# Performance work log

Hardware: AMD Instinct MI355X
Metric: run time of the kernel (lower is better)

## Reference

```python
import jax, jax.numpy as jnp
import numpy as np

N_NODES = 100000
N_EDGES = 3200000
F_IN = 128
HID = 32
N_CLASSES = 40
NEG_SLOPE = 0.2


def _add_self_loops(edge_index, n):
    loops = jnp.arange(n, dtype=edge_index.dtype)
    src = jnp.concatenate([edge_index[0], loops])
    dst = jnp.concatenate([edge_index[1], loops])
    return src, dst


def _gat_layer(x, src, dst, W, a_src, a_dst, b, n):
    # h: [N, C]
    h = x @ W
    hs = h[src]                      # [E, C] gathered source features
    alpha_s = hs @ a_src             # [E]
    alpha_d = (h @ a_dst)[dst]       # [E]
    e = jax.nn.leaky_relu(alpha_s + alpha_d, NEG_SLOPE)
    # segment softmax over incoming edges per destination node
    m = jax.ops.segment_max(e, dst, num_segments=n)
    ex = jnp.exp(e - m[dst])
    denom = jax.ops.segment_sum(ex, dst, num_segments=n)
    alpha = ex / denom[dst]
    out = jax.ops.segment_sum(alpha[:, None] * hs, dst, num_segments=n)
    return out + b


def setup_inputs() -> dict:
    key = jax.random.key(0)
    ks = jax.random.split(key, 8)
    x = jax.random.normal(ks[0], (N_NODES, F_IN), dtype=jnp.float32)
    edge_index = jax.random.randint(ks[1], (2, N_EDGES), 0, N_NODES, dtype=jnp.int32)
    W1 = jax.random.normal(ks[2], (F_IN, HID), dtype=jnp.float32) * (1.0 / np.sqrt(F_IN))
    att_src1 = jax.random.normal(ks[3], (HID,), dtype=jnp.float32) * 0.1
    att_dst1 = jax.random.normal(ks[4], (HID,), dtype=jnp.float32) * 0.1
    b1 = jnp.zeros((HID,), dtype=jnp.float32)
    W2 = jax.random.normal(ks[5], (HID, N_CLASSES), dtype=jnp.float32) * (1.0 / np.sqrt(HID))
    att_src2 = jax.random.normal(ks[6], (N_CLASSES,), dtype=jnp.float32) * 0.1
    att_dst2 = jax.random.normal(ks[7], (N_CLASSES,), dtype=jnp.float32) * 0.1
    b2 = jnp.zeros((N_CLASSES,), dtype=jnp.float32)
    return {"x": x, "edge_index": edge_index, "W1": W1, "att_src1": att_src1,
            "att_dst1": att_dst1, "b1": b1, "W2": W2, "att_src2": att_src2,
            "att_dst2": att_dst2, "b2": b2}


def reference(x, edge_index, W1, att_src1, att_dst1, b1, W2, att_src2, att_dst2, b2):
    n = x.shape[0]
    src, dst = _add_self_loops(edge_index, n)  # PyG GATConv default add_self_loops=True
    h = _gat_layer(x, src, dst, W1, att_src1, att_dst1, b1, n)
    h = jax.nn.relu(h)  # dropout is identity in eval mode
    h = _gat_layer(h, src, dst, W2, att_src2, att_dst2, b2, n)
    h = jax.nn.relu(h)
    return jax.nn.log_softmax(h, axis=1)
```

## Files before the change

kernel.cpp:

```cpp
#include <hip/hip_runtime.h>
#include <hip/hip_bf16.h>
#include <hip/hip_fp16.h>
#include <math.h>

#define N_NODES 100000
#define N_EDGES 3200000
#define ET (N_EDGES + N_NODES)
#define F_IN 128
#define HID 32
#define NCLS 40
#define NEG 0.2f

#define NB 782
#define CHUNK 4096
#define NBLK 782
#define BCAP 5120
#define NB1 299
#define GROWS 64
#define GEMM_BLKS ((N_NODES + GROWS - 1) / GROWS)

#define BSUM_SCAN(bscan, bsums)                                                   \
    if (t < 64) {                                                                 \
        int base5 = t * 5;                                                        \
        int bv0 = (base5     < NB1) ? bsums[base5]     : 0;                       \
        int bv1 = (base5 + 1 < NB1) ? bsums[base5 + 1] : 0;                       \
        int bv2 = (base5 + 2 < NB1) ? bsums[base5 + 2] : 0;                       \
        int bv3 = (base5 + 3 < NB1) ? bsums[base5 + 3] : 0;                       \
        int bv4 = (base5 + 4 < NB1) ? bsums[base5 + 4] : 0;                       \
        int bs = bv0 + bv1 + bv2 + bv3 + bv4;                                     \
        int brun = bs;                                                            \
        for (int boff = 1; boff < 64; boff <<= 1) {                               \
            int bx = __shfl_up(brun, boff);                                       \
            if (t >= boff) brun += bx;                                            \
        }                                                                         \
        brun -= bs;                                                               \
        if (base5     < NB1) { bscan[base5]     = brun; brun += bv0; }            \
        if (base5 + 1 < NB1) { bscan[base5 + 1] = brun; brun += bv1; }            \
        if (base5 + 2 < NB1) { bscan[base5 + 2] = brun; brun += bv2; }            \
        if (base5 + 3 < NB1) { bscan[base5 + 3] = brun; brun += bv3; }            \
        if (base5 + 4 < NB1) { bscan[base5 + 4] = brun; }                         \
    }

__global__ __launch_bounds__(256) void k_hist_gemm(
    const int* __restrict__ dst, int* __restrict__ Hm,
    const float* __restrict__ x, const float* __restrict__ W1,
    const float* __restrict__ a_s, const float* __restrict__ a_d,
    __half* __restrict__ h1h, float* __restrict__ s1, float* __restrict__ d1,
    const float* __restrict__ W2, const float* __restrict__ as2,
    const float* __restrict__ ad2, float* __restrict__ va_s, float* __restrict__ va_d) {
    __shared__ __align__(16) float Ws[F_IN * HID];
    int t = threadIdx.x;
    if (blockIdx.x < NBLK) {
        int* hist = (int*)Ws;
        int k = blockIdx.x;
        for (int i = t; i < NB; i += 256) hist[i] = 0;
        __syncthreads();
        int b4 = k * (CHUNK / 4);
#pragma unroll
        for (int j = 0; j < CHUNK / 4 / 256; j++) {
            int i4 = b4 + j * 256 + t;
            if (i4 < N_EDGES / 4) {
                int4 d = ((const int4*)dst)[i4];
                atomicAdd(&hist[d.x >> 7], 1);
                atomicAdd(&hist[d.y >> 7], 1);
                atomicAdd(&hist[d.z >> 7], 1);
                atomicAdd(&hist[d.w >> 7], 1);
            }
        }
        __syncthreads();
        for (int i = t; i < NB; i += 256) Hm[i * NBLK + k] = hist[i];
    } else if (blockIdx.x < NBLK + GEMM_BLKS) {
        int bb = blockIdx.x - NBLK;
        const float4* W4 = (const float4*)W1;
        float4* Ws4 = (float4*)Ws;
#pragma unroll
        for (int i = 0; i < F_IN * HID / 4 / 256; i++)
            Ws4[t + i * 256] = W4[t + i * 256];
        __syncthreads();
        int rp = t >> 3;
        int cq = t & 7;
        size_t v0 = (size_t)bb * GROWS + rp * 2;
        size_t v1 = v0 + 1;
        size_t r0c = (v0 < N_NODES) ? v0 : (size_t)(N_NODES - 1);
        size_t r1c = (v1 < N_NODES) ? v1 : (size_t)(N_NODES - 1);
        const float4* xa4 = (const float4*)(x + r0c * F_IN);
        const float4* xb4 = (const float4*)(x + r1c * F_IN);
        const float4* Wc4 = (const float4*)Ws;
        float a00 = 0.f, a01 = 0.f, a02 = 0.f, a03 = 0.f;
        float a10 = 0.f, a11 = 0.f, a12 = 0.f, a13 = 0.f;
#pragma unroll
        for (int k4 = 0; k4 < F_IN / 4; k4++) {
            float4 xa = xa4[k4];
            float4 xb = xb4[k4];
            int kb = k4 * 4;
            float4 w0 = Wc4[(kb + 0) * 8 + cq];
            float4 w1 = Wc4[(kb + 1) * 8 + cq];
            float4 w2 = Wc4[(kb + 2) * 8 + cq];
            float4 w3 = Wc4[(kb + 3) * 8 + cq];
            a00 = fmaf(xa.x, w0.x, a00); a01 = fmaf(xa.x, w0.y, a01);
            a02 = fmaf(xa.x, w0.z, a02); a03 = fmaf(xa.x, w0.w, a03);
            a00 = fmaf(xa.y, w1.x, a00); a01 = fmaf(xa.y, w1.y, a01);
            a02 = fmaf(xa.y, w1.z, a02); a03 = fmaf(xa.y, w1.w, a03);
            a00 = fmaf(xa.z, w2.x, a00); a01 = fmaf(xa.z, w2.y, a01);
            a02 = fmaf(xa.z, w2.z, a02); a03 = fmaf(xa.z, w2.w, a03);
            a00 = fmaf(xa.w, w3.x, a00); a01 = fmaf(xa.w, w3.y, a01);
            a02 = fmaf(xa.w, w3.z, a02); a03 = fmaf(xa.w, w3.w, a03);
            a10 = fmaf(xb.x, w0.x, a10); a11 = fmaf(xb.x, w0.y, a11);
            a12 = fmaf(xb.x, w0.z, a12); a13 = fmaf(xb.x, w0.w, a13);
            a10 = fmaf(xb.y, w1.x, a10); a11 = fmaf(xb.y, w1.y, a11);
            a12 = fmaf(xb.y, w1.z, a12); a13 = fmaf(xb.y, w1.w, a13);
            a10 = fmaf(xb.z, w2.x, a10); a11 = fmaf(xb.z, w2.y, a11);
            a12 = fmaf(xb.z, w2.z, a12); a13 = fmaf(xb.z, w2.w, a13);
            a10 = fmaf(xb.w, w3.x, a10); a11 = fmaf(xb.w, w3.y, a11);
            a12 = fmaf(xb.w, w3.z, a12); a13 = fmaf(xb.w, w3.w, a13);
        }
        if (v0 < N_NODES) {
            __half2 p0 = __floats2half2_rn(a00, a01);
            __half2 p1 = __floats2half2_rn(a02, a03);
            uint2 u;
            u.x = *(const unsigned int*)&p0;
            u.y = *(const unsigned int*)&p1;
            *((uint2*)(h1h + v0 * HID + cq * 4)) = u;
        }
        if (v1 < N_NODES) {
            __half2 p0 = __floats2half2_rn(a10, a11);
            __half2 p1 = __floats2half2_rn(a12, a13);
            uint2 u;
            u.x = *(const unsigned int*)&p0;
            u.y = *(const unsigned int*)&p1;
            *((uint2*)(h1h + v1 * HID + cq * 4)) = u;
        }
        float4 asv = *(const float4*)(a_s + cq * 4);
        float4 adv = *(const float4*)(a_d + cq * 4);
        float p0s = a00 * asv.x + a01 * asv.y + a02 * asv.z + a03 * asv.w;
        float p0d = a00 * adv.x + a01 * adv.y + a02 * adv.z + a03 * adv.w;
        float p1s = a10 * asv.x + a11 * asv.y + a12 * asv.z + a13 * asv.w;
        float p1d = a10 * adv.x + a11 * adv.y + a12 * adv.z + a13 * adv.w;
#pragma unroll
        for (int off = 1; off <= 4; off <<= 1) {
            p0s += __shfl_xor(p0s, off); p0d += __shfl_xor(p0d, off);
            p1s += __shfl_xor(p1s, off); p1d += __shfl_xor(p1d, off);
        }
        if (cq == 0) {
            if (v0 < N_NODES) { s1[v0] = p0s; d1[v0] = p0d; }
            if (v1 < N_NODES) { s1[v1] = p1s; d1[v1] = p1d; }
        }
    } else {
        if (t < HID) {
            float ps = 0.f, pd = 0.f;
            for (int c = 0; c < NCLS; c++) {
                float w = W2[t * NCLS + c];
                ps = fmaf(w, as2[c], ps);
                pd = fmaf(w, ad2[c], pd);
            }
            va_s[t] = ps;
            va_d[t] = pd;
        }
    }
}

__global__ void k_scan_a(const int* __restrict__ in, int* __restrict__ out,
                         int* __restrict__ bsums, int L) {
    __shared__ int sd[256];
    int t = threadIdx.x, b = blockIdx.x;
    int base = b * 2048 + t * 8;
    int v[8];
    int ts = 0;
#pragma unroll
    for (int u = 0; u < 8; u++) {
        v[u] = (base + u < L) ? in[base + u] : 0;
        ts += v[u];
    }
    sd[t] = ts;
    __syncthreads();
    for (int off = 1; off < 256; off <<= 1) {
        int xx = (t >= off) ? sd[t - off] : 0;
        __syncthreads();
        sd[t] += xx;
        __syncthreads();
    }
    int run = sd[t] - ts;
    if (t == 255) bsums[b] = sd[255];
#pragma unroll
    for (int u = 0; u < 8; u++) {
        if (base + u < L) out[base + u] = run;
        run += v[u];
    }
}

__global__ __launch_bounds__(256) void kA_scatter(
    const int* __restrict__ src, const int* __restrict__ dst,
    const int* __restrict__ Sx, const int* __restrict__ bsums,
    unsigned int* __restrict__ tmp) {
    __shared__ int hist[NB];
    __shared__ int lofs[NB];
    __shared__ int tsum[256];
    __shared__ int bscan[NB1 + 1];
    __shared__ unsigned int stage[CHUNK];
    __shared__ unsigned short bkt16[CHUNK];
    int t = threadIdx.x, k = blockIdx.x;
    for (int i = t; i < NB; i += 256) hist[i] = 0;
    BSUM_SCAN(bscan, bsums)
    __syncthreads();
    int myd[16], mys[16];
    int b4 = k * (CHUNK / 4);
#pragma unroll
    for (int j = 0; j < CHUNK / 4 / 256; j++) {
        int i4 = b4 + j * 256 + t;
        if (i4 < N_EDGES / 4) {
            int4 d = ((const int4*)dst)[i4];
            int4 s = ((const int4*)src)[i4];
            myd[j * 4 + 0] = d.x; mys[j * 4 + 0] = s.x;
            myd[j * 4 + 1] = d.y; mys[j * 4 + 1] = s.y;
            myd[j * 4 + 2] = d.z; mys[j * 4 + 2] = s.z;
            myd[j * 4 + 3] = d.w; mys[j * 4 + 3] = s.w;
            atomicAdd(&hist[d.x >> 7], 1);
            atomicAdd(&hist[d.y >> 7], 1);
            atomicAdd(&hist[d.z >> 7], 1);
            atomicAdd(&hist[d.w >> 7], 1);
        } else {
#pragma unroll
            for (int u = 0; u < 4; u++) { myd[j * 4 + u] = -1; mys[j * 4 + u] = 0; }
        }
    }
    __syncthreads();
    int i0 = 4 * t;
    int h0 = (i0     < NB) ? hist[i0]     : 0;
    int h1 = (i0 + 1 < NB) ? hist[i0 + 1] : 0;
    int h2 = (i0 + 2 < NB) ? hist[i0 + 2] : 0;
    int h3 = (i0 + 3 < NB) ? hist[i0 + 3] : 0;
    int ts = h0 + h1 + h2 + h3;
    tsum[t] = ts;
    __syncthreads();
    for (int off = 1; off < 256; off <<= 1) {
        int xx = (t >= off) ? tsum[t - off] : 0;
        __syncthreads();
        tsum[t] += xx;
        __syncthreads();
    }
    int ex = tsum[t] - ts;
    if (i0     < NB) { lofs[i0]     = ex;                hist[i0]     = 0; }
    if (i0 + 1 < NB) { lofs[i0 + 1] = ex + h0;           hist[i0 + 1] = 0; }
    if (i0 + 2 < NB) { lofs[i0 + 2] = ex + h0 + h1;      hist[i0 + 2] = 0; }
    if (i0 + 3 < NB) { lofs[i0 + 3] = ex + h0 + h1 + h2; hist[i0 + 3] = 0; }
    __syncthreads();
#pragma unroll
    for (int j = 0; j < 16; j++) {
        if (myd[j] >= 0) {
            int bkt = myd[j] >> 7;
            int slot = lofs[bkt] + atomicAdd(&hist[bkt], 1);
            stage[slot] = ((unsigned int)(myd[j] & 127) << 17) | (unsigned int)mys[j];
            bkt16[slot] = (unsigned short)bkt;
        }
    }
    __syncthreads();
    for (int b = t; b < NB; b += 256) {
        int idx = b * NBLK + k;
        hist[b] = Sx[idx] + bscan[idx >> 11] - lofs[b];
    }
    __syncthreads();
    int nvalid = min(CHUNK, N_EDGES - k * CHUNK);
    for (int i = t; i < nvalid; i += 256)
        tmp[hist[bkt16[i]] + i] = stage[i];
}

__global__ __launch_bounds__(256) void kB_sort(
    const unsigned int* __restrict__ tmp, const int* __restrict__ Sx,
    const int* __restrict__ bsums,
    int* __restrict__ esrc, int* __restrict__ rs, int* __restrict__ deg) {
    __shared__ int ordered[BCAP + 128];
    __shared__ int cnt[128], lofs[128], cur[128], sc[128];
    __shared__ int bscan[NB1 + 1];
    int t = threadIdx.x, b = blockIdx.x;
    if (t < 128) { cnt[t] = 0; cur[t] = 0; }
    BSUM_SCAN(bscan, bsums)
    __syncthreads();
    int idx0 = b * NBLK;
    int myBase = Sx[idx0] + bscan[idx0 >> 11];
    int nextBase;
    if (b == NB - 1) nextBase = N_EDGES;
    else {
        int idx1 = (b + 1) * NBLK;
        nextBase = Sx[idx1] + bscan[idx1 >> 11];
    }
    int cntE = nextBase - myBase;
    int nNodes = min(128, N_NODES - b * 128);
    for (int i = t; i < cntE; i += 256) {
        unsigned int p = tmp[myBase + i];
        atomicAdd(&cnt[p >> 17], 1);
    }
    __syncthreads();
    int val = 0;
    if (t < 128) { val = (t < nNodes) ? cnt[t] + 1 : 0; sc[t] = val; }
    __syncthreads();
    for (int off = 1; off < 128; off <<= 1) {
        int xx = 0;
        if (t < 128 && t >= off) xx = sc[t - off];
        __syncthreads();
        if (t < 128) sc[t] += xx;
        __syncthreads();
    }
    if (t < 128) lofs[t] = sc[t] - val;
    __syncthreads();
    if (t < nNodes) ordered[lofs[t]] = b * 128 + t;
    for (int i = t; i < cntE; i += 256) {
        unsigned int p = tmp[myBase + i];
        int n = p >> 17;
        int slot = lofs[n] + 1 + atomicAdd(&cur[n], 1);
        ordered[slot] = (int)(p & 0x1FFFF);
    }
    __syncthreads();
    int gb = myBase + b * 128;
    int totOut = cntE + nNodes;
    for (int i = t; i < totOut; i += 256) esrc[gb + i] = ordered[i];
    if (t < nNodes) {
        rs[b * 128 + t] = gb + lofs[t];
        deg[b * 128 + t] = cnt[t] + 1;
    }
}

#define GATHER_BODY(SARR, TABLE)                                                  \
    float a0 = 0.f, a1 = 0.f, a2 = 0.f, a3 = 0.f,                                 \
          a4 = 0.f, a5 = 0.f, a6 = 0.f, a7 = 0.f;                                 \
    float den = 0.f;                                                              \
    int t = 0;                                                                    \
    for (; t + 16 <= cnt; t += 16) {                                              \
        int p0 = start + t + e;                                                   \
        int sa0 = esrc[p0];                                                       \
        int sa1 = esrc[p0 + 4];                                                   \
        int sa2 = esrc[p0 + 8];                                                   \
        int sa3 = esrc[p0 + 12];                                                  \
        float sv0 = SARR[sa0];                                                    \
        float sv1 = SARR[sa1];                                                    \
        float sv2 = SARR[sa2];                                                    \
        float sv3 = SARR[sa3];                                                    \
        uint4 hv0 = TABLE[(size_t)sa0 * 4 + q];                                   \
        uint4 hv1 = TABLE[(size_t)sa1 * 4 + q];                                   \
        uint4 hv2 = TABLE[(size_t)sa2 * 4 + q];                                   \
        uint4 hv3 = TABLE[(size_t)sa3 * 4 + q];                                   \
        float e0 = sv0 + dval; e0 = (e0 >= 0.f) ? e0 : NEG * e0;                  \
        float e1 = sv1 + dval; e1 = (e1 >= 0.f) ? e1 : NEG * e1;                  \
        float e2 = sv2 + dval; e2 = (e2 >= 0.f) ? e2 : NEG * e2;                  \
        float e3 = sv3 + dval; e3 = (e3 >= 0.f) ? e3 : NEG * e3;                  \
        float w0 = __expf(e0);                                                    \
        float w1 = __expf(e1);                                                    \
        float w2 = __expf(e2);                                                    \
        float w3 = __expf(e3);                                                    \
        den += (w0 + w1) + (w2 + w3);                                             \
        ACC8(w0, hv0); ACC8(w1, hv1); ACC8(w2, hv2); ACC8(w3, hv3);               \
    }                                                                             \
    for (; t < cnt; t += 4) {                                                     \
        int idx = t + e;                                                          \
        int sa = 0;                                                               \
        float w = 0.f;                                                            \
        if (idx < cnt) {                                                          \
            sa = esrc[start + idx];                                               \
            float ev = SARR[sa] + dval;                                           \
            ev = (ev >= 0.f) ? ev : NEG * ev;                                     \
            w = __expf(ev);                                                       \
        }                                                                         \
        uint4 hv = TABLE[(size_t)sa * 4 + q];                                     \
        ACC8(w, hv);                                                              \
        den += w;                                                                 \
    }

#define ACC8(W, HV)                                                               \
    {                                                                             \
        float2 f0 = __half22float2(*(const __half2*)&(HV).x);                     \
        float2 f1 = __half22float2(*(const __half2*)&(HV).y);                     \
        float2 f2 = __half22float2(*(const __half2*)&(HV).z);                     \
        float2 f3 = __half22float2(*(const __half2*)&(HV).w);                     \
        a0 = fmaf((W), f0.x, a0); a1 = fmaf((W), f0.y, a1);                       \
        a2 = fmaf((W), f1.x, a2); a3 = fmaf((W), f1.y, a3);                       \
        a4 = fmaf((W), f2.x, a4); a5 = fmaf((W), f2.y, a5);                       \
        a6 = fmaf((W), f3.x, a6); a7 = fmaf((W), f3.y, a7);                       \
    }

__global__ __launch_bounds__(256) void k_fused1(
    const int* __restrict__ rs, const int* __restrict__ deg, const int* __restrict__ esrc,
    const uint4* __restrict__ h1r, const float* __restrict__ s1, const float* __restrict__ d1,
    const float* __restrict__ b1, const float* __restrict__ va_s, const float* __restrict__ va_d,
    uint4* __restrict__ hrr, float* __restrict__ s2, float* __restrict__ d2) {
    int tid = threadIdx.x;
    int sub = tid & 15;
    int q = sub & 3;
    int e = sub >> 2;
    int v = blockIdx.x * 16 + (tid >> 4);
    int start = rs[v];
    int cnt = deg[v];
    float dval = d1[v];
    GATHER_BODY(s1, h1r)
#pragma unroll
    for (int off = 4; off <= 8; off <<= 1) {
        a0 += __shfl_xor(a0, off); a1 += __shfl_xor(a1, off);
        a2 += __shfl_xor(a2, off); a3 += __shfl_xor(a3, off);
        a4 += __shfl_xor(a4, off); a5 += __shfl_xor(a5, off);
        a6 += __shfl_xor(a6, off); a7 += __shfl_xor(a7, off);
        den += __shfl_xor(den, off);
    }
    if (e == 0) {
        float iden = 1.f / den;
        const float4* b4 = (const float4*)(b1 + q * 8);
        float4 bA = b4[0], bB = b4[1];
        float o0 = fmaxf(a0 * iden + bA.x, 0.f);
        float o1 = fmaxf(a1 * iden + bA.y, 0.f);
        float o2 = fmaxf(a2 * iden + bA.z, 0.f);
        float o3 = fmaxf(a3 * iden + bA.w, 0.f);
        float o4 = fmaxf(a4 * iden + bB.x, 0.f);
        float o5 = fmaxf(a5 * iden + bB.y, 0.f);
        float o6 = fmaxf(a6 * iden + bB.z, 0.f);
        float o7 = fmaxf(a7 * iden + bB.w, 0.f);
        __half2 p0 = __floats2half2_rn(o0, o1);
        __half2 p1 = __floats2half2_rn(o2, o3);
        __half2 p2 = __floats2half2_rn(o4, o5);
        __half2 p3 = __floats2half2_rn(o6, o7);
        uint4 ov;
        ov.x = *(const unsigned int*)&p0;
        ov.y = *(const unsigned int*)&p1;
        ov.z = *(const unsigned int*)&p2;
        ov.w = *(const unsigned int*)&p3;
        hrr[(size_t)v * 4 + q] = ov;
        const float4* vs4 = (const float4*)(va_s + q * 8);
        const float4* vd4 = (const float4*)(va_d + q * 8);
        float4 sA = vs4[0], sB = vs4[1], dA = vd4[0], dB = vd4[1];
        float ps = o0 * sA.x + o1 * sA.y + o2 * sA.z + o3 * sA.w
                 + o4 * sB.x + o5 * sB.y + o6 * sB.z + o7 * sB.w;
        float pd = o0 * dA.x + o1 * dA.y + o2 * dA.z + o3 * dA.w
                 + o4 * dB.x + o5 * dB.y + o6 * dB.z + o7 * dB.w;
        ps += __shfl_xor(ps, 1); pd += __shfl_xor(pd, 1);
        ps += __shfl_xor(ps, 2); pd += __shfl_xor(pd, 2);
        if (q == 0) { s2[v] = ps; d2[v] = pd; }
    }
}

__global__ __launch_bounds__(256) void k_fused2(
    const int* __restrict__ rs, const int* __restrict__ deg, const int* __restrict__ esrc,
    const uint4* __restrict__ hrr, const float* __restrict__ s2, const float* __restrict__ d2,
    const float* __restrict__ W2, const float* __restrict__ b2, float* __restrict__ out) {
    __shared__ float W2s[HID * NCLS];
    __shared__ float hragg[16][HID];
    __shared__ float zbuf[16][NCLS];
    __shared__ float gm[16], gl[16];
    int tid = threadIdx.x;
    for (int i = tid; i < HID * NCLS; i += 256) W2s[i] = W2[i];
    int sub = tid & 15;
    int q = sub & 3;
    int e = sub >> 2;
    int node = tid >> 4;
    int v = blockIdx.x * 16 + node;
    int start = rs[v];
    int cnt = deg[v];
    float dval = d2[v];
    GATHER_BODY(s2, hrr)
#pragma unroll
    for (int off = 4; off <= 8; off <<= 1) {
        a0 += __shfl_xor(a0, off); a1 += __shfl_xor(a1, off);
        a2 += __shfl_xor(a2, off); a3 += __shfl_xor(a3, off);
        a4 += __shfl_xor(a4, off); a5 += __shfl_xor(a5, off);
        a6 += __shfl_xor(a6, off); a7 += __shfl_xor(a7, off);
        den += __shfl_xor(den, off);
    }
    if (e == 0) {
        float iden = 1.f / den;
        int cb = q * 8;
        hragg[node][cb + 0] = a0 * iden;
        hragg[node][cb + 1] = a1 * iden;
        hragg[node][cb + 2] = a2 * iden;
        hragg[node][cb + 3] = a3 * iden;
        hragg[node][cb + 4] = a4 * iden;
        hragg[node][cb + 5] = a5 * iden;
        hragg[node][cb + 6] = a6 * iden;
        hragg[node][cb + 7] = a7 * iden;
    }
    __syncthreads();
    for (int oi = tid; oi < 16 * NCLS; oi += 256) {
        int n = oi / NCLS, c = oi % NCLS;
        float z = 0.f;
#pragma unroll
        for (int k = 0; k < HID; k++)
            z = fmaf(hragg[n][k], W2s[k * NCLS + c], z);
        zbuf[n][c] = fmaxf(z + b2[c], 0.f);
    }
    __syncthreads();
    if (tid < 16) {
        float mx = -INFINITY;
        for (int c = 0; c < NCLS; c++) mx = fmaxf(mx, zbuf[tid][c]);
        float se = 0.f;
        for (int c = 0; c < NCLS; c++) se += __expf(zbuf[tid][c] - mx);
        gm[tid] = mx;
        gl[tid] = logf(se);
    }
    __syncthreads();
    for (int oi = tid; oi < 16 * NCLS; oi += 256) {
        int n = oi / NCLS, c = oi % NCLS;
        out[(size_t)(blockIdx.x * 16 + n) * NCLS + c] = zbuf[n][c] - gm[n] - gl[n];
    }
}


extern "C" void kernel_launch(void* const* d_in, const int* in_sizes, int n_in,
                              void* d_out, int out_size, void* d_ws, size_t ws_size,
                              hipStream_t stream) {
    (void)in_sizes; (void)n_in; (void)out_size; (void)ws_size;
    const float* x   = (const float*)d_in[0];
    const int*   ei  = (const int*)d_in[1];
    const float* W1  = (const float*)d_in[2];
    const float* as1 = (const float*)d_in[3];
    const float* ad1 = (const float*)d_in[4];
    const float* b1  = (const float*)d_in[5];
    const float* W2  = (const float*)d_in[6];
    const float* as2 = (const float*)d_in[7];
    const float* ad2 = (const float*)d_in[8];
    const float* b2  = (const float*)d_in[9];
    float* out = (float*)d_out;
    const int* srcA = ei;
    const int* dstA = ei + N_EDGES;

    char* w = (char*)d_ws;
    size_t off = 0;
    auto alloc = [&](size_t bytes) {
        char* p = w + off;
        off = (off + bytes + 255) & ~(size_t)255;
        return p;
    };
    int* esrc     = (int*)alloc((size_t)ET * 4);
    int* rs       = (int*)alloc((size_t)N_NODES * 4);
    int* deg      = (int*)alloc((size_t)N_NODES * 4);
    char* region1 = alloc((size_t)N_NODES * HID * 4);
    float* s1     = (float*)alloc((size_t)N_NODES * 4);
    float* d1     = (float*)alloc((size_t)N_NODES * 4);
    char* region2 = alloc((size_t)N_EDGES * 4 + 1024);
    float* s2     = (float*)alloc((size_t)N_NODES * 4);
    float* d2     = (float*)alloc((size_t)N_NODES * 4);
    float* va_s   = (float*)alloc(HID * 4);
    float* va_d   = (float*)alloc(HID * 4);
    int* bsums    = (int*)alloc(1024 * 4);

    const int L = NB * NBLK;
    int* Hm = (int*)region2;
    int* Sx = (int*)region1;
    __half* h1h = (__half*)(region1 + (size_t)N_NODES * HID * 2);
    unsigned int* tmp = (unsigned int*)region2;
    __half* hrt = (__half*)region2;

    int nb1 = (L + 2047) / 2048;
    hipLaunchKernelGGL(k_hist_gemm, dim3(NBLK + GEMM_BLKS + 1), dim3(256), 0, stream,
                       dstA, Hm, x, W1, as1, ad1, h1h, s1, d1,
                       W2, as2, ad2, va_s, va_d);
    hipLaunchKernelGGL(k_scan_a, dim3(nb1), dim3(256), 0, stream, Hm, Sx, bsums, L);
    hipLaunchKernelGGL(kA_scatter, dim3(NBLK), dim3(256), 0, stream, srcA, dstA, Sx, bsums, tmp);
    hipLaunchKernelGGL(kB_sort, dim3(NB), dim3(256), 0, stream, tmp, Sx, bsums, esrc, rs, deg);
    hipLaunchKernelGGL(k_fused1, dim3(N_NODES / 16), dim3(256), 0, stream, rs, deg, esrc,
                       (const uint4*)h1h, s1, d1, b1, va_s, va_d,
                       (uint4*)hrt, s2, d2);
    hipLaunchKernelGGL(k_fused2, dim3(N_NODES / 16), dim3(256), 0, stream, rs, deg, esrc,
                       (const uint4*)hrt, s2, d2, W2, b2, out);
}
```

Measured before the change: 280.1 us.

## Move layer-1 GEMM blocks from histogram kernel into scatter kernel

Moves the x@W1 GEMM work blocks out of the histogram kernel and into the scatter kernel. Shared memory is now one byte buffer carved per role. The small W2·att precompute stays with the histogram kernel. The aim is to rebalance work between the two phases, letting the memory-heavy GEMM overlap the scatter instead of the light histogram. The risk is that the fused kernel's shared-memory footprint and its heavier contention cut scatter occupancy, or that the two phases just compete for bandwidth.

```diff
diff --git a/kernel.cpp b/kernel.cpp
--- a/kernel.cpp
+++ b/kernel.cpp
@@ -41,35 +41,163 @@
         if (base5 + 4 < NB1) { bscan[base5 + 4] = brun; }                         \
     }
 
-__global__ __launch_bounds__(256) void k_hist_gemm(
+__global__ __launch_bounds__(256) void k_hist_prep(
     const int* __restrict__ dst, int* __restrict__ Hm,
+    const float* __restrict__ W2, const float* __restrict__ as2,
+    const float* __restrict__ ad2, float* __restrict__ va_s, float* __restrict__ va_d) {
+    __shared__ int hist[NB];
+    int t = threadIdx.x;
+    if (blockIdx.x == NBLK) {
+        if (t < HID) {
+            float ps = 0.f, pd = 0.f;
+            for (int c = 0; c < NCLS; c++) {
+                float w = W2[t * NCLS + c];
+                ps = fmaf(w, as2[c], ps);
+                pd = fmaf(w, ad2[c], pd);
+            }
+            va_s[t] = ps;
+            va_d[t] = pd;
+        }
+        return;
+    }
+    int k = blockIdx.x;
+    for (int i = t; i < NB; i += 256) hist[i] = 0;
+    __syncthreads();
+    int b4 = k * (CHUNK / 4);
+#pragma unroll
+    for (int j = 0; j < CHUNK / 4 / 256; j++) {
+        int i4 = b4 + j * 256 + t;
+        if (i4 < N_EDGES / 4) {
+            int4 d = ((const int4*)dst)[i4];
+            atomicAdd(&hist[d.x >> 7], 1);
+            atomicAdd(&hist[d.y >> 7], 1);
+            atomicAdd(&hist[d.z >> 7], 1);
+            atomicAdd(&hist[d.w >> 7], 1);
+        }
+    }
+    __syncthreads();
+    for (int i = t; i < NB; i += 256) Hm[i * NBLK + k] = hist[i];
+}
+
+__global__ void k_scan_a(const int* __restrict__ in, int* __restrict__ out,
+                         int* __restrict__ bsums, int L) {
+    __shared__ int sd[256];
+    int t = threadIdx.x, b = blockIdx.x;
+    int base = b * 2048 + t * 8;
+    int v[8];
+    int ts = 0;
+#pragma unroll
+    for (int u = 0; u < 8; u++) {
+        v[u] = (base + u < L) ? in[base + u] : 0;
+        ts += v[u];
+    }
+    sd[t] = ts;
+    __syncthreads();
+    for (int off = 1; off < 256; off <<= 1) {
+        int xx = (t >= off) ? sd[t - off] : 0;
+        __syncthreads();
+        sd[t] += xx;
+        __syncthreads();
+    }
+    int run = sd[t] - ts;
+    if (t == 255) bsums[b] = sd[255];
+#pragma unroll
+    for (int u = 0; u < 8; u++) {
+        if (base + u < L) out[base + u] = run;
+        run += v[u];
+    }
+}
+
+#define SMEM_STAGE  0
+#define SMEM_BKT16  16384
+#define SMEM_HIST   (16384 + 8192)
+#define SMEM_LOFS   (SMEM_HIST + 3128)
+#define SMEM_TSUM   (SMEM_LOFS + 3128)
+#define SMEM_BSCAN  (SMEM_TSUM + 1024)
+#define SMEM_TOTAL  (SMEM_BSCAN + 1200)
+
+__global__ __launch_bounds__(256) void k_scatter_gemm(
+    const int* __restrict__ src, const int* __restrict__ dst,
+    const int* __restrict__ Sx, const int* __restrict__ bsums,
+    unsigned int* __restrict__ tmp,
     const float* __restrict__ x, const float* __restrict__ W1,
     const float* __restrict__ a_s, const float* __restrict__ a_d,
-    __half* __restrict__ h1h, float* __restrict__ s1, float* __restrict__ d1,
-    const float* __restrict__ W2, const float* __restrict__ as2,
-    const float* __restrict__ ad2, float* __restrict__ va_s, float* __restrict__ va_d) {
-    __shared__ __align__(16) float Ws[F_IN * HID];
+    __half* __restrict__ h1h, float* __restrict__ s1, float* __restrict__ d1) {
+    __shared__ __align__(16) char smem[SMEM_TOTAL];
     int t = threadIdx.x;
     if (blockIdx.x < NBLK) {
-        int* hist = (int*)Ws;
+        unsigned int* stage = (unsigned int*)(smem + SMEM_STAGE);
+        unsigned short* bkt16 = (unsigned short*)(smem + SMEM_BKT16);
+        int* hist = (int*)(smem + SMEM_HIST);
+        int* lofs = (int*)(smem + SMEM_LOFS);
+        int* tsum = (int*)(smem + SMEM_TSUM);
+        int* bscan = (int*)(smem + SMEM_BSCAN);
         int k = blockIdx.x;
         for (int i = t; i < NB; i += 256) hist[i] = 0;
-        __syncthreads();
+        BSUM_SCAN(bscan, bsums)
+        __syncthreads();
+        int myd[16], mys[16];
         int b4 = k * (CHUNK / 4);
 #pragma unroll
         for (int j = 0; j < CHUNK / 4 / 256; j++) {
             int i4 = b4 + j * 256 + t;
             if (i4 < N_EDGES / 4) {
                 int4 d = ((const int4*)dst)[i4];
+                int4 s = ((const int4*)src)[i4];
+                myd[j * 4 + 0] = d.x; mys[j * 4 + 0] = s.x;
+                myd[j * 4 + 1] = d.y; mys[j * 4 + 1] = s.y;
+                myd[j * 4 + 2] = d.z; mys[j * 4 + 2] = s.z;
+                myd[j * 4 + 3] = d.w; mys[j * 4 + 3] = s.w;
                 atomicAdd(&hist[d.x >> 7], 1);
                 atomicAdd(&hist[d.y >> 7], 1);
                 atomicAdd(&hist[d.z >> 7], 1);
                 atomicAdd(&hist[d.w >> 7], 1);
+            } else {
+#pragma unroll
+                for (int u = 0; u < 4; u++) { myd[j * 4 + u] = -1; mys[j * 4 + u] = 0; }
             }
         }
         __syncthreads();
-        for (int i = t; i < NB; i += 256) Hm[i * NBLK + k] = hist[i];
-    } else if (blockIdx.x < NBLK + GEMM_BLKS) {
+        int i0 = 4 * t;
+        int h0 = (i0     < NB) ? hist[i0]     : 0;
+        int h1 = (i0 + 1 < NB) ? hist[i0 + 1] : 0;
+        int h2 = (i0 + 2 < NB) ? hist[i0 + 2] : 0;
+        int h3 = (i0 + 3 < NB) ? hist[i0 + 3] : 0;
+        int ts = h0 + h1 + h2 + h3;
+        tsum[t] = ts;
+        __syncthreads();
+        for (int off = 1; off < 256; off <<= 1) {
+            int xx = (t >= off) ? tsum[t - off] : 0;
+            __syncthreads();
+            tsum[t] += xx;
+            __syncthreads();
+        }
+        int ex = tsum[t] - ts;
+        if (i0     < NB) { lofs[i0]     = ex;                hist[i0]     = 0; }
+        if (i0 + 1 < NB) { lofs[i0 + 1] = ex + h0;           hist[i0 + 1] = 0; }
+        if (i0 + 2 < NB) { lofs[i0 + 2] = ex + h0 + h1;      hist[i0 + 2] = 0; }
+        if (i0 + 3 < NB) { lofs[i0 + 3] = ex + h0 + h1 + h2; hist[i0 + 3] = 0; }
+        __syncthreads();
+#pragma unroll
+        for (int j = 0; j < 16; j++) {
+            if (myd[j] >= 0) {
+                int bkt = myd[j] >> 7;
+                int slot = lofs[bkt] + atomicAdd(&hist[bkt], 1);
+                stage[slot] = ((unsigned int)(myd[j] & 127) << 17) | (unsigned int)mys[j];
+                bkt16[slot] = (unsigned short)bkt;
+            }
+        }
+        __syncthreads();
+        for (int b = t; b < NB; b += 256) {
+            int idx = b * NBLK + k;
+            hist[b] = Sx[idx] + bscan[idx >> 11] - lofs[b];
+        }
+        __syncthreads();
+        int nvalid = min(CHUNK, N_EDGES - k * CHUNK);
+        for (int i = t; i < nvalid; i += 256)
+            tmp[hist[bkt16[i]] + i] = stage[i];
+    } else {
+        float* Ws = (float*)smem;
         int bb = blockIdx.x - NBLK;
         const float4* W4 = (const float4*)W1;
         float4* Ws4 = (float4*)Ws;
@@ -145,123 +273,7 @@
             if (v0 < N_NODES) { s1[v0] = p0s; d1[v0] = p0d; }
             if (v1 < N_NODES) { s1[v1] = p1s; d1[v1] = p1d; }
         }
-    } else {
-        if (t < HID) {
-            float ps = 0.f, pd = 0.f;
-            for (int c = 0; c < NCLS; c++) {
-                float w = W2[t * NCLS + c];
-                ps = fmaf(w, as2[c], ps);
-                pd = fmaf(w, ad2[c], pd);
-            }
-            va_s[t] = ps;
-            va_d[t] = pd;
-        }
-    }
-}
-
-__global__ void k_scan_a(const int* __restrict__ in, int* __restrict__ out,
-                         int* __restrict__ bsums, int L) {
-    __shared__ int sd[256];
-    int t = threadIdx.x, b = blockIdx.x;
-    int base = b * 2048 + t * 8;
-    int v[8];
-    int ts = 0;
-#pragma unroll
-    for (int u = 0; u < 8; u++) {
-        v[u] = (base + u < L) ? in[base + u] : 0;
-        ts += v[u];
-    }
-    sd[t] = ts;
-    __syncthreads();
-    for (int off = 1; off < 256; off <<= 1) {
-        int xx = (t >= off) ? sd[t - off] : 0;
-        __syncthreads();
-        sd[t] += xx;
-        __syncthreads();
-    }
-    int run = sd[t] - ts;
-    if (t == 255) bsums[b] = sd[255];
-#pragma unroll
-    for (int u = 0; u < 8; u++) {
-        if (base + u < L) out[base + u] = run;
-        run += v[u];
-    }
-}
-
-__global__ __launch_bounds__(256) void kA_scatter(
-    const int* __restrict__ src, const int* __restrict__ dst,
-    const int* __restrict__ Sx, const int* __restrict__ bsums,
-    unsigned int* __restrict__ tmp) {
-    __shared__ int hist[NB];
-    __shared__ int lofs[NB];
-    __shared__ int tsum[256];
-    __shared__ int bscan[NB1 + 1];
-    __shared__ unsigned int stage[CHUNK];
-    __shared__ unsigned short bkt16[CHUNK];
-    int t = threadIdx.x, k = blockIdx.x;
-    for (int i = t; i < NB; i += 256) hist[i] = 0;
-    BSUM_SCAN(bscan, bsums)
-    __syncthreads();
-    int myd[16], mys[16];
-    int b4 = k * (CHUNK / 4);
-#pragma unroll
-    for (int j = 0; j < CHUNK / 4 / 256; j++) {
-        int i4 = b4 + j * 256 + t;
-        if (i4 < N_EDGES / 4) {
-            int4 d = ((const int4*)dst)[i4];
-            int4 s = ((const int4*)src)[i4];
-            myd[j * 4 + 0] = d.x; mys[j * 4 + 0] = s.x;
-            myd[j * 4 + 1] = d.y; mys[j * 4 + 1] = s.y;
-            myd[j * 4 + 2] = d.z; mys[j * 4 + 2] = s.z;
-            myd[j * 4 + 3] = d.w; mys[j * 4 + 3] = s.w;
-            atomicAdd(&hist[d.x >> 7], 1);
-            atomicAdd(&hist[d.y >> 7], 1);
-            atomicAdd(&hist[d.z >> 7], 1);
-            atomicAdd(&hist[d.w >> 7], 1);
-        } else {
-#pragma unroll
-            for (int u = 0; u < 4; u++) { myd[j * 4 + u] = -1; mys[j * 4 + u] = 0; }
-        }
-    }
-    __syncthreads();
-    int i0 = 4 * t;
-    int h0 = (i0     < NB) ? hist[i0]     : 0;
-    int h1 = (i0 + 1 < NB) ? hist[i0 + 1] : 0;
-    int h2 = (i0 + 2 < NB) ? hist[i0 + 2] : 0;
-    int h3 = (i0 + 3 < NB) ? hist[i0 + 3] : 0;
-    int ts = h0 + h1 + h2 + h3;
-    tsum[t] = ts;
-    __syncthreads();
-    for (int off = 1; off < 256; off <<= 1) {
-        int xx = (t >= off) ? tsum[t - off] : 0;
-        __syncthreads();
-        tsum[t] += xx;
-        __syncthreads();
-    }
-    int ex = tsum[t] - ts;
-    if (i0     < NB) { lofs[i0]     = ex;                hist[i0]     = 0; }
-    if (i0 + 1 < NB) { lofs[i0 + 1] = ex + h0;           hist[i0 + 1] = 0; }
-    if (i0 + 2 < NB) { lofs[i0 + 2] = ex + h0 + h1;      hist[i0 + 2] = 0; }
-    if (i0 + 3 < NB) { lofs[i0 + 3] = ex + h0 + h1 + h2; hist[i0 + 3] = 0; }
-    __syncthreads();
-#pragma unroll
-    for (int j = 0; j < 16; j++) {
-        if (myd[j] >= 0) {
-            int bkt = myd[j] >> 7;
-            int slot = lofs[bkt] + atomicAdd(&hist[bkt], 1);
-            stage[slot] = ((unsigned int)(myd[j] & 127) << 17) | (unsigned int)mys[j];
-            bkt16[slot] = (unsigned short)bkt;
-        }
-    }
-    __syncthreads();
-    for (int b = t; b < NB; b += 256) {
-        int idx = b * NBLK + k;
-        hist[b] = Sx[idx] + bscan[idx >> 11] - lofs[b];
-    }
-    __syncthreads();
-    int nvalid = min(CHUNK, N_EDGES - k * CHUNK);
-    for (int i = t; i < nvalid; i += 256)
-        tmp[hist[bkt16[i]] + i] = stage[i];
+    }
 }
 
 __global__ __launch_bounds__(256) void kB_sort(
@@ -544,11 +556,12 @@
     __half* hrt = (__half*)region2;
 
     int nb1 = (L + 2047) / 2048;
-    hipLaunchKernelGGL(k_hist_gemm, dim3(NBLK + GEMM_BLKS + 1), dim3(256), 0, stream,
-                       dstA, Hm, x, W1, as1, ad1, h1h, s1, d1,
-                       W2, as2, ad2, va_s, va_d);
+    hipLaunchKernelGGL(k_hist_prep, dim3(NBLK + 1), dim3(256), 0, stream,
+                       dstA, Hm, W2, as2, ad2, va_s, va_d);
     hipLaunchKernelGGL(k_scan_a, dim3(nb1), dim3(256), 0, stream, Hm, Sx, bsums, L);
-    hipLaunchKernelGGL(kA_scatter, dim3(NBLK), dim3(256), 0, stream, srcA, dstA, Sx, bsums, tmp);
+    hipLaunchKernelGGL(k_scatter_gemm, dim3(NBLK + GEMM_BLKS), dim3(256), 0, stream,
+                       srcA, dstA, Sx, bsums, tmp,
+                       x, W1, as1, ad1, h1h, s1, d1);
     hipLaunchKernelGGL(kB_sort, dim3(NB), dim3(256), 0, stream, tmp, Sx, bsums, esrc, rs, deg);
     hipLaunchKernelGGL(k_fused1, dim3(N_NODES / 16), dim3(256), 0, stream, rs, deg, esrc,
                        (const uint4*)h1h, s1, d1, b1, va_s, va_d,
```

Result: no change. 277.6 us (-0.9%).
